# Kernel optimization log

Measured on AMD Instinct MI355X. Metric: run time of the kernel, lower is better.

Reference implementation:

```python
import jax, jax.numpy as jnp
import numpy as np
from jax import lax

# Config (matches init_kwargs)
B, CIN, H, W = 32, 256, 56, 56
COUT, KS, STRIDE, PAD, GROUPS = 256, 3, 1, 1, 2
CG_IN = CIN // GROUPS            # 128
OUT_F = COUT // GROUPS           # 128 per-group out features
IN_F = CG_IN * KS * KS           # 1152 per-group in features
Q = (IN_F * OUT_F // 4) * GROUPS # 73728 quadruplets total
TAU = 1.0

# All six 2-of-4 masking patterns (as in the torch module)
_MASK_PATTERNS = np.array([[0.,0.,1.,1.],[0.,1.,0.,1.],[0.,1.,1.,0.],
                           [1.,0.,0.,1.],[1.,0.,1.,0.],[1.,1.,0.,0.]], dtype=np.float32)


def setup_inputs() -> dict:
    key = jax.random.key(0)
    k1, k2, k3, k4 = jax.random.split(key, 4)
    x = jax.random.normal(k1, (B, CIN, H, W), dtype=jnp.float32)
    # per-group weight blocks, xavier-ish scale
    Ws = jax.random.normal(k2, (GROUPS, OUT_F, IN_F), dtype=jnp.float32) * 0.03
    choice_weights = jax.random.normal(k3, (Q, 6), dtype=jnp.float32)
    # gumbel noise: -log(Exp(1)) ~ Gumbel(0,1), matching -empty.exponential_().log()
    gumbels = -jnp.log(jax.random.exponential(k4, (Q, 6), dtype=jnp.float32))
    masking_patterns = jnp.asarray(_MASK_PATTERNS)
    return {"x": x, "Ws": Ws, "choice_weights": choice_weights,
            "gumbels": gumbels, "masking_patterns": masking_patterns}


def _hard_gumbel_softmax(logits, gumbels, tau):
    # straight-through hard gumbel softmax over last dim
    y_soft = jax.nn.softmax((logits + gumbels) / tau, axis=-1)
    idx = jnp.argmax(y_soft, axis=-1)
    y_hard = jax.nn.one_hot(idx, logits.shape[-1], dtype=logits.dtype)
    return y_hard - lax.stop_gradient(y_soft) + y_soft


def reference(x, Ws, choice_weights, gumbels, masking_patterns):
    # 1) sample 2:4 mask per quadruplet via hard gumbel-softmax choice over 6 patterns
    choice = _hard_gumbel_softmax(choice_weights, gumbels, TAU)   # (Q, 6)
    mask = choice @ masking_patterns                              # (Q, 4)
    mask = mask.reshape(GROUPS, OUT_F, IN_F)                      # quadruplets tile W row-major
    Wm = Ws * mask                                                # (G, OUT_F, IN_F)

    # 2) im2col (torch Unfold ordering: channel-major, then kh, kw)
    patches = lax.conv_general_dilated_patches(
        x, filter_shape=(KS, KS), window_strides=(STRIDE, STRIDE),
        padding=[(PAD, PAD), (PAD, PAD)])                         # (B, CIN*KS*KS, Ho, Wo)
    Ho = (H + 2 * PAD - KS) // STRIDE + 1
    Wo = (W + 2 * PAD - KS) // STRIDE + 1
    L = Ho * Wo
    # channel-major ordering => group g occupies contiguous IN_F rows
    patches = patches.reshape(B, GROUPS, IN_F, L)                 # (B, G, IN_F, L)

    # 3) per-group masked GEMM, no bias (use_bias=False)
    y = jnp.einsum('goi,bgil->bgol', Wm, patches)                 # (B, G, OUT_F, L)
    return y.reshape(B, COUT, Ho, Wo)
```

## Files before the change

### kernel.cpp

```cpp
#include <hip/hip_runtime.h>


#define INF   1152
#define HO    56
#define LOUT  3136
#define XP    58

typedef __attribute__((ext_vector_type(8))) short bf16x8;
typedef __attribute__((ext_vector_type(4))) float f32x4;

__device__ __forceinline__ unsigned short f2bf(float f) {
  union { float f; unsigned u; } v; v.f = f;
  unsigned r = v.u + 0x7fffu + ((v.u >> 16) & 1u);
  return (unsigned short)(r >> 16);
}

__device__ __forceinline__ void async_load16(const void* g, void* l) {
  __builtin_amdgcn_global_load_lds(
      (const __attribute__((address_space(1))) void*)g,
      (__attribute__((address_space(3))) void*)l, 16, 0, 0);
}

__global__ __launch_bounds__(256) void prep_kernel(
    const float* __restrict__ x, const float* __restrict__ Ws,
    const float* __restrict__ cw, const float* __restrict__ gb,
    const float* __restrict__ pat,
    unsigned short* __restrict__ Xt, unsigned short* __restrict__ Wt) {
  __shared__ float lds[56 * 129];
  const int t   = threadIdx.x;
  const int bid = blockIdx.x;

  if (bid >= 3712) {
    int idx = (bid - 3712) * 256 + t;
    int c   = idx & 127;
    int of  = (idx >> 7) & 127;
    int gt  = idx >> 14;
    int g   = gt / 9;
    int tap = gt - g * 9;
    int e   = ((g << 7) + of) * INF + c * 9 + tap;
    int q   = e >> 2, pos = e & 3;
    const float* cq = cw + q * 6;
    const float* gq = gb + q * 6;
    float best = cq[0] + gq[0]; int bi = 0;
    #pragma unroll
    for (int j = 1; j < 6; ++j) {
      float v2 = cq[j] + gq[j];
      if (v2 > best) { best = v2; bi = j; }
    }
    Wt[idx] = f2bf(Ws[e] * pat[bi * 4 + pos]);
    return;
  }

  const int bg  = bid / 58;
  const int ihp = bid - bg * 58;
  uint4* dst = (uint4*)(Xt + ((bg * XP + ihp) * XP) * 128);
  if (ihp == 0 || ihp == XP - 1) {
    const uint4 z = {0u, 0u, 0u, 0u};
    for (int i = t; i < XP * 16; i += 256) dst[i] = z;
    return;
  }
  const int ih = ihp - 1;
  const float4* src = (const float4*)(x + (bg * 128) * LOUT + ih * HO);
  for (int i = t; i < 128 * 14; i += 256) {
    int c = i / 14, seg = i - c * 14;
    float4 v = src[c * (LOUT / 4) + seg];
    float* row = &lds[(seg * 4) * 129 + c];
    row[0]       = v.x;
    row[129]     = v.y;
    row[2 * 129] = v.z;
    row[3 * 129] = v.w;
  }
  __syncthreads();
  for (int i = t; i < XP * 16; i += 256) {
    int iwp = i >> 4, oct = i & 15;
    uint4 val = {0u, 0u, 0u, 0u};
    if (iwp != 0 && iwp != XP - 1) {
      const float* s = &lds[(iwp - 1) * 129 + (oct << 3)];
      val.x = (unsigned)f2bf(s[0]) | ((unsigned)f2bf(s[1]) << 16);
      val.y = (unsigned)f2bf(s[2]) | ((unsigned)f2bf(s[3]) << 16);
      val.z = (unsigned)f2bf(s[4]) | ((unsigned)f2bf(s[5]) << 16);
      val.w = (unsigned)f2bf(s[6]) | ((unsigned)f2bf(s[7]) << 16);
    }
    dst[i] = val;
  }
}

__global__ __launch_bounds__(256, 4) void conv_mfma_kernel(
    const unsigned short* __restrict__ Wt, const unsigned short* __restrict__ Xt,
    float* __restrict__ out) {
  __shared__ __align__(16) unsigned short sA[128 * 64];
  __shared__ __align__(16) unsigned short sB[128 * 64];
  const int t  = threadIdx.x;
  const int ln = t & 63, wv = t >> 6;
  const int wm = wv >> 1, wn = wv & 1;
  const int col = ln & 15, kq = ln >> 4, c7 = col & 7;

  const int lid   = blockIdx.y * 25 + blockIdx.x;
  const int v     = (lid & 7) * 200 + (lid >> 3);
  const int bg    = v / 25;
  const int tileN = v - bg * 25;
  const int g     = bg & 1;
  const int l0    = tileN << 7;

  const int r8 = ln >> 3;
  const int ch = (ln & 7) ^ r8;
  int arow[4], brow[4];
  #pragma unroll
  for (int i = 0; i < 4; ++i) {
    const int rr = (wv << 5) + (i << 3) + r8;
    arow[i] = (rr << 7) + (ch << 3);
    int ll = l0 + rr;
    if (ll > LOUT - 1) ll = LOUT - 1;
    int oh = ll / HO, ow = ll - oh * HO;
    brow[i] = ((bg * XP + oh) * XP + ow) * 128 + (ch << 3);
  }

  f32x4 acc[4][4];
  #pragma unroll
  for (int i = 0; i < 4; ++i)
    #pragma unroll
    for (int j = 0; j < 4; ++j) acc[i][j] = (f32x4){0.f, 0.f, 0.f, 0.f};

  for (int tap = 0; tap < 9; ++tap) {
    const int th = tap / 3, tw = tap - th * 3;
    const int bTap = (th * XP + tw) << 7;
    const int aTap = (g * 9 + tap) << 14;
    #pragma unroll 1
    for (int kc = 0; kc < 2; ++kc) {
      const int c0 = kc << 6;
      __syncthreads();
      #pragma unroll
      for (int i = 0; i < 4; ++i) {
        const int lb = ((wv << 5) + (i << 3)) << 6;
        async_load16(Wt + aTap + c0 + arow[i], &sA[lb]);
        async_load16(Xt + bTap + c0 + brow[i], &sB[lb]);
      }
      __syncthreads();
      #pragma unroll
      for (int kh = 0; kh < 2; ++kh) {
        const int pk = (((kh << 2) + kq) ^ c7) << 3;
        bf16x8 af[4], bfr[4];
        #pragma unroll
        for (int mi = 0; mi < 4; ++mi)
          af[mi] = *(const bf16x8*)&sA[(((wm << 6) + (mi << 4) + col) << 6) + pk];
        #pragma unroll
        for (int ni = 0; ni < 4; ++ni)
          bfr[ni] = *(const bf16x8*)&sB[(((wn << 6) + (ni << 4) + col) << 6) + pk];
        #pragma unroll
        for (int mi = 0; mi < 4; ++mi)
          #pragma unroll
          for (int ni = 0; ni < 4; ++ni)
            acc[mi][ni] = __builtin_amdgcn_mfma_f32_16x16x32_bf16(
                af[mi], bfr[ni], acc[mi][ni], 0, 0, 0);
      }
    }
  }

  const int rowq = kq << 2;
  #pragma unroll
  for (int mi = 0; mi < 4; ++mi) {
    #pragma unroll
    for (int ni = 0; ni < 4; ++ni) {
      const int l = l0 + (wn << 6) + (ni << 4) + col;
      if (l < LOUT) {
        #pragma unroll
        for (int r = 0; r < 4; ++r) {
          const int of = (wm << 6) + (mi << 4) + rowq + r;
          out[(bg * 128 + of) * LOUT + l] = acc[mi][ni][r];
        }
      }
    }
  }
}

extern "C" void kernel_launch(void* const* d_in, const int* in_sizes, int n_in,
                              void* d_out, int out_size, void* d_ws, size_t ws_size,
                              hipStream_t stream) {
  const float* x   = (const float*)d_in[0];
  const float* Ws  = (const float*)d_in[1];
  const float* cw  = (const float*)d_in[2];
  const float* gb  = (const float*)d_in[3];
  const float* pat = (const float*)d_in[4];
  float* out = (float*)d_out;

  unsigned short* Wt = (unsigned short*)d_ws;
  unsigned short* Xt = (unsigned short*)((char*)d_ws + (1 << 20));

  prep_kernel<<<4864, 256, 0, stream>>>(x, Ws, cw, gb, pat, Xt, Wt);
  conv_mfma_kernel<<<dim3(25, 64), 256, 0, stream>>>(Wt, Xt, out);
}
```

Baseline: 253.6 us.

## Double-buffer LDS tiles to prefetch next K-step during MFMA compute

Result: slower. 272.1 us (+7.3%).

```diff
diff --git a/kernel.cpp b/kernel.cpp
--- a/kernel.cpp
+++ b/kernel.cpp
@@ -85,11 +85,18 @@
   }
 }
 
-__global__ __launch_bounds__(256, 4) void conv_mfma_kernel(
+__device__ __forceinline__ void step_offs(int s, int g, int& aOff, int& bOff) {
+  const int tap = s >> 1, kc = s & 1;
+  const int th = tap / 3, tw = tap - th * 3;
+  aOff = ((g * 9 + tap) << 14) + (kc << 6);
+  bOff = ((th * XP + tw) << 7) + (kc << 6);
+}
+
+__global__ __launch_bounds__(256, 2) void conv_mfma_kernel(
     const unsigned short* __restrict__ Wt, const unsigned short* __restrict__ Xt,
     float* __restrict__ out) {
-  __shared__ __align__(16) unsigned short sA[128 * 64];
-  __shared__ __align__(16) unsigned short sB[128 * 64];
+  __shared__ __align__(16) unsigned short sA[2][128 * 64];
+  __shared__ __align__(16) unsigned short sB[2][128 * 64];
   const int t  = threadIdx.x;
   const int ln = t & 63, wv = t >> 6;
   const int wm = wv >> 1, wn = wv & 1;
@@ -104,7 +111,7 @@
 
   const int r8 = ln >> 3;
   const int ch = (ln & 7) ^ r8;
-  int arow[4], brow[4];
+  int arow[4], brow[4], lbs[4];
   #pragma unroll
   for (int i = 0; i < 4; ++i) {
     const int rr = (wv << 5) + (i << 3) + r8;
@@ -113,6 +120,7 @@
     if (ll > LOUT - 1) ll = LOUT - 1;
     int oh = ll / HO, ow = ll - oh * HO;
     brow[i] = ((bg * XP + oh) * XP + ow) * 128 + (ch << 3);
+    lbs[i]  = ((wv << 5) + (i << 3)) << 6;
   }
 
   f32x4 acc[4][4];
@@ -121,39 +129,47 @@
     #pragma unroll
     for (int j = 0; j < 4; ++j) acc[i][j] = (f32x4){0.f, 0.f, 0.f, 0.f};
 
-  for (int tap = 0; tap < 9; ++tap) {
-    const int th = tap / 3, tw = tap - th * 3;
-    const int bTap = (th * XP + tw) << 7;
-    const int aTap = (g * 9 + tap) << 14;
-    #pragma unroll 1
-    for (int kc = 0; kc < 2; ++kc) {
-      const int c0 = kc << 6;
-      __syncthreads();
+  {
+    int aOff, bOff;
+    step_offs(0, g, aOff, bOff);
+    #pragma unroll
+    for (int i = 0; i < 4; ++i) {
+      async_load16(Wt + aOff + arow[i], &sA[0][lbs[i]]);
+      async_load16(Xt + bOff + brow[i], &sB[0][lbs[i]]);
+    }
+  }
+  __syncthreads();
+
+  #pragma unroll 1
+  for (int s = 0; s < 18; ++s) {
+    const int buf = s & 1;
+    if (s < 17) {
+      int aOff, bOff;
+      step_offs(s + 1, g, aOff, bOff);
       #pragma unroll
       for (int i = 0; i < 4; ++i) {
-        const int lb = ((wv << 5) + (i << 3)) << 6;
-        async_load16(Wt + aTap + c0 + arow[i], &sA[lb]);
-        async_load16(Xt + bTap + c0 + brow[i], &sB[lb]);
+        async_load16(Wt + aOff + arow[i], &sA[buf ^ 1][lbs[i]]);
+        async_load16(Xt + bOff + brow[i], &sB[buf ^ 1][lbs[i]]);
       }
-      __syncthreads();
-      #pragma unroll
-      for (int kh = 0; kh < 2; ++kh) {
-        const int pk = (((kh << 2) + kq) ^ c7) << 3;
-        bf16x8 af[4], bfr[4];
-        #pragma unroll
-        for (int mi = 0; mi < 4; ++mi)
-          af[mi] = *(const bf16x8*)&sA[(((wm << 6) + (mi << 4) + col) << 6) + pk];
+    }
+    #pragma unroll
+    for (int kh = 0; kh < 2; ++kh) {
+      const int pk = (((kh << 2) + kq) ^ c7) << 3;
+      bf16x8 af[4], bfr[4];
+      #pragma unroll
+      for (int mi = 0; mi < 4; ++mi)
+        af[mi] = *(const bf16x8*)&sA[buf][(((wm << 6) + (mi << 4) + col) << 6) + pk];
+      #pragma unroll
+      for (int ni = 0; ni < 4; ++ni)
+        bfr[ni] = *(const bf16x8*)&sB[buf][(((wn << 6) + (ni << 4) + col) << 6) + pk];
+      #pragma unroll
+      for (int mi = 0; mi < 4; ++mi)
         #pragma unroll
         for (int ni = 0; ni < 4; ++ni)
-          bfr[ni] = *(const bf16x8*)&sB[(((wn << 6) + (ni << 4) + col) << 6) + pk];
-        #pragma unroll
-        for (int mi = 0; mi < 4; ++mi)
-          #pragma unroll
-          for (int ni = 0; ni < 4; ++ni)
-            acc[mi][ni] = __builtin_amdgcn_mfma_f32_16x16x32_bf16(
-                af[mi], bfr[ni], acc[mi][ni], 0, 0, 0);
-      }
-    }
+          acc[mi][ni] = __builtin_amdgcn_mfma_f32_16x16x32_bf16(
+              af[mi], bfr[ni], acc[mi][ni], 0, 0, 0);
+    }
+    __syncthreads();
   }
 
   const int rowq = kq << 2;
```
